# Performance work log

Measured on AMD Instinct MI355X. Metric: run time of the kernel, lower is better.

## Reference

```python
import jax, jax.numpy as jnp
import numpy as np

DIM = 1024
DEPTH = 3
BATCH = 8
SEQ = DIM  # module requires seq_len == dim for the residual add to broadcast


def setup_inputs() -> dict:
    key = jax.random.key(0)
    k1, k2, k3, k4 = jax.random.split(key, 4)
    x = jax.random.normal(k1, (BATCH, SEQ, DIM), dtype=jnp.float32)
    # torch.nn.Linear(dim, 3*dim): weight [3*dim, dim], bias [3*dim]
    Wqkv = jax.random.normal(k2, (3 * DIM, DIM), dtype=jnp.float32) * (1.0 / np.sqrt(DIM))
    bqkv = jax.random.normal(k3, (3 * DIM,), dtype=jnp.float32) * 0.01
    # self.w: Parameter of shape [depth, dim, dim], init randn
    w = jax.random.normal(k4, (DEPTH, DIM, DIM), dtype=jnp.float32)
    return {"x": x, "Wqkv": Wqkv, "bqkv": bqkv, "w": w}


def reference(x, Wqkv, bqkv, w):
    # qkv projection then chunk into q, k, v along last dim
    qkv = x @ Wqkv.T + bqkv                      # [B, S, 3*dim]
    q, k, v = jnp.split(qkv, 3, axis=-1)         # each [B, S, dim]
    scale = 1.0 / (q.shape[-1] ** 0.5)
    # sum over depth of (q @ w[i]) @ k^T, accumulated onto v
    # einsum contracts d (dim), e (dim), and sums over n (depth) in one pass
    scores = jnp.einsum('bsd,nde,bte->bst', q, w, k)  # [B, S, S]; requires S == dim
    return v + scores * scale
```

## Files before the change

kernel.cpp:

```cpp
#include <hip/hip_runtime.h>
#include <hip/hip_bf16.h>
#include <stdint.h>

typedef __bf16 bf16_t;
typedef __bf16 bf16x8 __attribute__((ext_vector_type(8)));
typedef __bf16 bf16x4 __attribute__((ext_vector_type(4)));
typedef float  f32x4  __attribute__((ext_vector_type(4)));

#define DIM   1024
#define BATCH 8
#define SCALE 0.03125f


__device__ __forceinline__ float rowdot_bf16(const bf16_t* __restrict__ row,
                                             const float* __restrict__ vec, int lane) {
    float s = 0.f;
#pragma unroll
    for (int c = 0; c < 2; ++c) {
        const int d0 = (lane + c * 64) * 8;
        const bf16x8 v = *reinterpret_cast<const bf16x8*>(row + d0);
#pragma unroll
        for (int e = 0; e < 8; ++e) s += vec[d0 + e] * (float)v[e];
    }
#pragma unroll
    for (int off = 32; off; off >>= 1) s += __shfl_down(s, off);
    return s;
}

__device__ __forceinline__ void cvt4(const float* __restrict__ in,
                                     bf16_t* __restrict__ out, int i) {
    const float4 v = reinterpret_cast<const float4*>(in)[i];
    bf16x4 o;
    o.x = (bf16_t)v.x; o.y = (bf16_t)v.y; o.z = (bf16_t)v.z; o.w = (bf16_t)v.w;
    reinterpret_cast<bf16x4*>(out)[i] = o;
}

__device__ __forceinline__ void gemm_sk(const bf16_t* __restrict__ A, const bf16_t* __restrict__ B,
                                        float* __restrict__ oP, int s, int tid,
                                        bf16_t* As, bf16_t* Bs)
{
    const int wave = tid >> 6, lane = tid & 63;
    const int bm = (s >> 5) * 128;
    const int bn = ((s >> 2) & 7) * 128;
    const int kb = (s & 3) * 256;
    float* outP  = oP + (long)(s & 3) * 1048576;
    const int wr = wave >> 1, wc = wave & 1;
    const int lhi = lane >> 4, llo = lane & 15;

    f32x4 acc[4][4];
    const f32x4 fz = {0.f, 0.f, 0.f, 0.f};
#pragma unroll
    for (int i = 0; i < 4; ++i)
#pragma unroll
        for (int j = 0; j < 4; ++j) acc[i][j] = fz;

    for (int k0 = 0; k0 < 256; k0 += 32) {
#pragma unroll
        for (int i = 0; i < 2; ++i) {
            const int c  = wave * 128 + i * 64 + lane;
            const int r  = c >> 2;
            const int cc = (c & 3) << 3;
            const long ga = (long)(bm + r) * 1024 + kb + k0 + cc;
            const long gb = (long)(bn + r) * 1024 + kb + k0 + cc;
            const int lbase = (wave * 128 + i * 64) << 3;
            __builtin_amdgcn_global_load_lds(
                (const __attribute__((address_space(1))) uint32_t*)(A + ga),
                (__attribute__((address_space(3))) uint32_t*)(&As[lbase]), 16, 0, 0);
            __builtin_amdgcn_global_load_lds(
                (const __attribute__((address_space(1))) uint32_t*)(B + gb),
                (__attribute__((address_space(3))) uint32_t*)(&Bs[lbase]), 16, 0, 0);
        }
        __syncthreads();

        bf16x8 af[4], bfr[4];
#pragma unroll
        for (int mi = 0; mi < 4; ++mi)
            af[mi] = *reinterpret_cast<const bf16x8*>(&As[(wr * 64 + mi * 16 + llo) * 32 + lhi * 8]);
#pragma unroll
        for (int ni = 0; ni < 4; ++ni)
            bfr[ni] = *reinterpret_cast<const bf16x8*>(&Bs[(wc * 64 + ni * 16 + llo) * 32 + lhi * 8]);
#pragma unroll
        for (int mi = 0; mi < 4; ++mi)
#pragma unroll
            for (int ni = 0; ni < 4; ++ni)
                acc[mi][ni] = __builtin_amdgcn_mfma_f32_16x16x32_bf16(af[mi], bfr[ni], acc[mi][ni], 0, 0, 0);
        __syncthreads();
    }

#pragma unroll
    for (int mi = 0; mi < 4; ++mi) {
        const int r0 = bm + wr * 64 + mi * 16 + lhi * 4;
#pragma unroll
        for (int ni = 0; ni < 4; ++ni) {
            const int cg = bn + wc * 64 + ni * 16 + llo;
            const f32x4 v = acc[mi][ni];
#pragma unroll
            for (int j = 0; j < 4; ++j)
                outP[(long)(r0 + j) * 1024 + cg] = v[j];
        }
    }
}

__global__ __launch_bounds__(256)
void k_prep(const float* __restrict__ Wqkv, const float* __restrict__ w,
            bf16_t* __restrict__ weff, bf16_t* __restrict__ wtb,
            bf16_t* __restrict__ wqt, bf16_t* __restrict__ wkt)
{
    __shared__ float tile[32][33];
    const int b = blockIdx.x;
    if (b < 1024) {
        const int t  = b;
        const int tx = threadIdx.x & 31, ty = threadIdx.x >> 5;
        const int d0 = (t & 31) * 32, e0 = (t >> 5) * 32;
#pragma unroll
        for (int r = 0; r < 4; ++r) {
            const int d = d0 + r * 8 + ty;
            const int e = e0 + tx;
            const float sum =
                w[d * 1024 + e] + w[1048576 + d * 1024 + e] + w[2097152 + d * 1024 + e];
            tile[r * 8 + ty][tx] = sum;
            weff[(long)d * 1024 + e] = (bf16_t)sum;
        }
        __syncthreads();
#pragma unroll
        for (int r = 0; r < 4; ++r) {
            const int e = e0 + r * 8 + ty;
            const int d = d0 + tx;
            wtb[(long)e * 1024 + d] = (bf16_t)tile[tx][r * 8 + ty];
        }
    } else {
        const bool isQ = (b < 2048);
        const int t  = b - (isQ ? 1024 : 2048);
        const float* src = isQ ? Wqkv : (Wqkv + 1048576);
        bf16_t* dst = isQ ? wqt : wkt;
        const int tx = threadIdx.x & 31, ty = threadIdx.x >> 5;
        const int e0 = (t & 31) * 32, d0 = (t >> 5) * 32;
#pragma unroll
        for (int r = 0; r < 4; ++r)
            tile[r * 8 + ty][tx] = src[(long)(e0 + r * 8 + ty) * 1024 + d0 + tx];
        __syncthreads();
#pragma unroll
        for (int r = 0; r < 4; ++r)
            dst[(long)(d0 + r * 8 + ty) * 1024 + e0 + tx] = (bf16_t)tile[tx][r * 8 + ty];
    }
}

__global__ __launch_bounds__(256)
void k_midA(const bf16_t* __restrict__ wkt, const bf16_t* __restrict__ weff,
            const bf16_t* __restrict__ wtb, const float* __restrict__ bqkv,
            const float* __restrict__ x, bf16_t* __restrict__ xb,
            float* __restrict__ pX1, float* __restrict__ h1, float* __restrict__ h2)
{
    __shared__ __align__(16) bf16_t As[128 * 32];
    __shared__ __align__(16) bf16_t Bs[128 * 32];
    const int b = blockIdx.x;
    if (b < 256) {
        gemm_sk(wkt, weff, pX1, b, threadIdx.x, As, Bs);
        return;
    }
    if (b < 768) {
        const int wave = threadIdx.x >> 6, lane = threadIdx.x & 63;
        const int r = (b - 256) * 4 + wave;
        if (r < 1024) {
            const float s = rowdot_bf16(weff + (long)r * 1024, bqkv + 1024, lane);
            if (lane == 0) h1[r] = s;
        } else {
            const float s = rowdot_bf16(wtb + (long)(r - 1024) * 1024, bqkv, lane);
            if (lane == 0) h2[r - 1024] = s;
        }
        return;
    }
    cvt4(x, xb, (b - 768) * 256 + threadIdx.x);
}

__global__ __launch_bounds__(256)
void k_cvtA(const float* __restrict__ p, bf16_t* __restrict__ X1b,
            const bf16_t* __restrict__ wqt, const bf16_t* __restrict__ wkt,
            const float* __restrict__ h1, const float* __restrict__ h2,
            const float* __restrict__ bqkv,
            float* __restrict__ u, float* __restrict__ w2, float* __restrict__ cO)
{
    const int b = blockIdx.x;
    if (b < 1024) {
        const int i = b * 256 + threadIdx.x;
        const f32x4* rp = reinterpret_cast<const f32x4*>(p);
        const f32x4 a0 = rp[i], a1 = rp[i + 262144], a2 = rp[i + 524288], a3 = rp[i + 786432];
        bf16x4 o;
        o.x = (bf16_t)(a0.x + a1.x + a2.x + a3.x);
        o.y = (bf16_t)(a0.y + a1.y + a2.y + a3.y);
        o.z = (bf16_t)(a0.z + a1.z + a2.z + a3.z);
        o.w = (bf16_t)(a0.w + a1.w + a2.w + a3.w);
        reinterpret_cast<bf16x4*>(X1b)[i] = o;
    } else if (b < 1536) {
        const int wave = threadIdx.x >> 6, lane = threadIdx.x & 63;
        const int rr = (b - 1024) * 4 + wave;
        if (rr < 1024) {
            const float s = rowdot_bf16(wqt + (long)rr * 1024, h1, lane);
            if (lane == 0) u[rr] = s;
        } else {
            const float s = rowdot_bf16(wkt + (long)(rr - 1024) * 1024, h2, lane);
            if (lane == 0) w2[rr - 1024] = s;
        }
    } else {
        if (threadIdx.x < 64) {
            float s = 0.f;
            for (int i = threadIdx.x; i < 1024; i += 64) s += bqkv[i] * h1[i];
#pragma unroll
            for (int off = 32; off; off >>= 1) s += __shfl_down(s, off);
            if (threadIdx.x == 0) cO[0] = s;
        }
    }
}

__global__ __launch_bounds__(256)
void k_midB(const bf16_t* __restrict__ X1b, const bf16_t* __restrict__ wqt,
            float* __restrict__ pMT, const bf16_t* __restrict__ xb,
            const float* __restrict__ u, const float* __restrict__ w2,
            const float* __restrict__ cO, const float* __restrict__ Wqkv,
            bf16_t* __restrict__ wvb,
            float* __restrict__ RU, float* __restrict__ RW)
{
    __shared__ __align__(16) bf16_t As[128 * 32];
    __shared__ __align__(16) bf16_t Bs[128 * 32];
    const int b = blockIdx.x;
    if (b < 256) {
        gemm_sk(X1b, wqt, pMT, b, threadIdx.x, As, Bs);
        return;
    }
    if (b < 2304) {
        const int wave = threadIdx.x >> 6, lane = threadIdx.x & 63;
        const int s = (b - 256) * 4 + wave;
        const bf16_t* row = xb + (long)s * 1024;
        float s1 = 0.f, s2 = 0.f;
#pragma unroll
        for (int c = 0; c < 2; ++c) {
            const int d0 = (lane + c * 64) * 8;
            const bf16x8 v = *reinterpret_cast<const bf16x8*>(row + d0);
#pragma unroll
            for (int e = 0; e < 8; ++e) {
                const float f = (float)v[e];
                s1 += u[d0 + e] * f;
                s2 += w2[d0 + e] * f;
            }
        }
#pragma unroll
        for (int off = 32; off; off >>= 1) { s1 += __shfl_down(s1, off); s2 += __shfl_down(s2, off); }
        if (lane == 0) {
            RU[s] = SCALE * (s1 + cO[0]);
            RW[s] = SCALE * s2;
        }
        return;
    }
    cvt4(Wqkv + 2097152, wvb, (b - 2304) * 256 + threadIdx.x);
}

__global__ __launch_bounds__(256)
void k_cvtS(const float* __restrict__ p, bf16_t* __restrict__ out) {
    const int i = blockIdx.x * 256 + threadIdx.x;
    const f32x4* rp = reinterpret_cast<const f32x4*>(p);
    const f32x4 a0 = rp[i], a1 = rp[i + 262144], a2 = rp[i + 524288], a3 = rp[i + 786432];
    bf16x4 o;
    o.x = (bf16_t)(SCALE * (a0.x + a1.x + a2.x + a3.x));
    o.y = (bf16_t)(SCALE * (a0.y + a1.y + a2.y + a3.y));
    o.z = (bf16_t)(SCALE * (a0.z + a1.z + a2.z + a3.z));
    o.w = (bf16_t)(SCALE * (a0.w + a1.w + a2.w + a3.w));
    reinterpret_cast<bf16x4*>(out)[i] = o;
}

#define GLOAD(SRC, DST) __builtin_amdgcn_global_load_lds( \
    (const __attribute__((address_space(1))) uint32_t*)(SRC), \
    (__attribute__((address_space(3))) uint32_t*)(DST), 16, 0, 0)

template<int MODE>
__global__ __launch_bounds__(512, 2)
void k_db2(const bf16_t* __restrict__ A1, const bf16_t* __restrict__ A2,
           const bf16_t* __restrict__ B1, const bf16_t* __restrict__ B2,
           const float* __restrict__ RUv, const float* __restrict__ RWv,
           const float* __restrict__ bv,
           bf16_t* __restrict__ oT, float* __restrict__ oF)
{
    constexpr int SLOT = 32768;
    constexpr int NTT  = (MODE == 0) ? 16 : 32;
    __shared__ __align__(16) unsigned char slds[2 * SLOT];

    const int tid  = threadIdx.x;
    const int wave = tid >> 6, lane = tid & 63;
    const int wm = wave >> 2, wn = wave & 3;
    const int llo = lane & 15, lhi = lane >> 4;

    int bm, bn, z = 0;
    const int nw = ((int)blockIdx.x & 7) * 64 + ((int)blockIdx.x >> 3);
    if (MODE == 0) {
        bm = (nw >> 3) * 128;
        bn = (nw & 7) * 128;
    } else {
        z = nw >> 6;
        const int r = nw & 63;
        bm = (r >> 3) * 128; bn = (r & 7) * 128;
    }
    const long zo = (long)z << 20;

    const bf16_t *sA1[2], *sB1[2], *sA2[2], *sB2[2];
    int dA[2], dB[2];
#pragma unroll
    for (int j = 0; j < 2; ++j) {
        const int C = j * 512 + tid;
        const int r = C >> 3, u = (C & 7) ^ (r & 7);
        const long aoff = (long)(bm + r) * 1024 + (u << 3);
        const long boff = (long)(bn + r) * 1024 + (u << 3);
        sA1[j] = A1 + zo + aoff;  dA[j] = C << 4;
        sB1[j] = B1 + zo + boff;  dB[j] = 16384 + (C << 4);
        if (MODE == 1) { sA2[j] = A2 + zo + aoff; sB2[j] = B2 + boff; }
    }

    auto stage = [&](int tt) {
        unsigned char* s = &slds[(tt & 1) * SLOT];
        const long ko = (long)(tt & 15) << 6;
        const bool hB = (MODE == 1) && (tt >= 16);
#pragma unroll
        for (int j = 0; j < 2; ++j) {
            GLOAD((hB ? sA2[j] : sA1[j]) + ko, s + dA[j]);
            GLOAD((hB ? sB2[j] : sB1[j]) + ko, s + dB[j]);
        }
    };

    f32x4 acc[4][2];
    const f32x4 fz = {0.f, 0.f, 0.f, 0.f};
#pragma unroll
    for (int i = 0; i < 4; ++i)
#pragma unroll
        for (int j = 0; j < 2; ++j) acc[i][j] = fz;

    stage(0);

    for (int t = 0; t < NTT; ++t) {
        if (t + 1 < NTT) {
            stage(t + 1);
            asm volatile("s_waitcnt vmcnt(4)" ::: "memory");
        } else {
            asm volatile("s_waitcnt vmcnt(0)" ::: "memory");
        }
        __builtin_amdgcn_s_barrier();

        const unsigned char* sb = &slds[(t & 1) * SLOT];
#pragma unroll
        for (int ks = 0; ks < 2; ++ks) {
            bf16x8 af[4], bfv[2];
#pragma unroll
            for (int mi = 0; mi < 4; ++mi) {
                const int r = wm * 64 + mi * 16 + llo;
                af[mi] = *reinterpret_cast<const bf16x8*>(
                    sb + r * 128 + ((((ks << 2) | lhi) ^ (r & 7)) << 4));
            }
#pragma unroll
            for (int ni = 0; ni < 2; ++ni) {
                const int r = wn * 32 + ni * 16 + llo;
                bfv[ni] = *reinterpret_cast<const bf16x8*>(
                    sb + 16384 + r * 128 + ((((ks << 2) | lhi) ^ (r & 7)) << 4));
            }
            __builtin_amdgcn_s_setprio(1);
#pragma unroll
            for (int mi = 0; mi < 4; ++mi)
#pragma unroll
                for (int ni = 0; ni < 2; ++ni)
                    acc[mi][ni] = __builtin_amdgcn_mfma_f32_16x16x32_bf16(
                        af[mi], bfv[ni], acc[mi][ni], 0, 0, 0);
            __builtin_amdgcn_s_setprio(0);
        }
        asm volatile("s_waitcnt lgkmcnt(0)" ::: "memory");
        __builtin_amdgcn_s_barrier();
    }

#pragma unroll
    for (int mi = 0; mi < 4; ++mi) {
        const int lr0 = bm + wm * 64 + mi * 16 + lhi * 4;
#pragma unroll
        for (int ni = 0; ni < 2; ++ni) {
            const int cg = bn + wn * 32 + ni * 16 + llo;
            const f32x4 v = acc[mi][ni];
            if (MODE == 0) {
#pragma unroll
                for (int j = 0; j < 4; ++j)
                    oT[(long)(lr0 + j) * 1024 + cg] = (bf16_t)v[j];
            } else {
                const float cterm = RWv[z * 1024 + cg] + bv[cg];
#pragma unroll
                for (int j = 0; j < 4; ++j) {
                    const int lr = lr0 + j;
                    oF[zo + (long)lr * 1024 + cg] = v[j] + RUv[z * 1024 + lr] + cterm;
                }
            }
        }
    }
}
#undef GLOAD

extern "C" void kernel_launch(void* const* d_in, const int* in_sizes, int n_in,
                              void* d_out, int out_size, void* d_ws, size_t ws_size,
                              hipStream_t stream) {
    const float* x    = (const float*)d_in[0];
    const float* Wqkv = (const float*)d_in[1];
    const float* bqkv = (const float*)d_in[2];
    const float* w    = (const float*)d_in[3];
    float* out = (float*)d_out;

    char* ws = (char*)d_ws;
    bf16_t* xb   = (bf16_t*)ws;
    float*  pbig = (float*) (ws + (16l << 20));
    bf16_t* tsb  = (bf16_t*)(ws + (16l << 20));
    bf16_t* weff = (bf16_t*)(ws + (32l << 20));
    bf16_t* wtb  = (bf16_t*)(ws + (34l << 20));
    bf16_t* wqt  = (bf16_t*)(ws + (36l << 20));
    bf16_t* wkt  = (bf16_t*)(ws + (38l << 20));
    bf16_t* wvb  = (bf16_t*)(ws + (40l << 20));
    bf16_t* X1b  = (bf16_t*)(ws + (42l << 20));
    bf16_t* MTb  = (bf16_t*)(ws + (44l << 20));
    char*   sm   = ws + (46l << 20);
    float* h1 = (float*)sm;
    float* h2 = (float*)(sm + 4096);
    float* u  = (float*)(sm + 8192);
    float* w2 = (float*)(sm + 12288);
    float* cO = (float*)(sm + 16384);
    float* RU = (float*)(sm + 20480);
    float* RW = (float*)(sm + 53248);
    if (ws_size < (size_t)(54l << 20) + 65536) return;

    k_prep<<<3072, 256, 0, stream>>>(Wqkv, w, weff, wtb, wqt, wkt);

    k_midA<<<8960, 256, 0, stream>>>(wkt, weff, wtb, bqkv, x, xb, pbig, h1, h2);

    k_cvtA<<<1537, 256, 0, stream>>>(pbig, X1b, wqt, wkt, h1, h2, bqkv, u, w2, cO);

    k_midB<<<3328, 256, 0, stream>>>(X1b, wqt, pbig, xb, u, w2, cO, Wqkv, wvb, RU, RW);

    k_cvtS<<<1024, 256, 0, stream>>>(pbig, MTb);

    k_db2<0><<<512, 512, 0, stream>>>(xb, nullptr, MTb, nullptr,
                                      nullptr, nullptr, nullptr, tsb, nullptr);

    k_db2<1><<<512, 512, 0, stream>>>(tsb, xb, xb, wvb,
                                      RU, RW, bqkv + 2048, nullptr, out);
}
```

Measured before the change: 107.7 us.

## Merge five prep kernels into one cooperative persistent kernel with grid syncs

Replaces the k_prep, k_midA, k_cvtA, k_midB and k_cvtS launches with a single 256-block cooperative kernel. Each block loops over its share of the work, and grid.sync() separates the dependent phases. This removes four kernel launch gaps and their tail effects. The cost is lower parallelism in the elementwise and transpose phases, which previously used thousands of blocks, plus the overhead of each grid barrier.

After: 238.6 us. 2.22x slower.

```diff
diff --git a/kernel.cpp b/kernel.cpp
--- a/kernel.cpp
+++ b/kernel.cpp
@@ -1,6 +1,9 @@
 #include <hip/hip_runtime.h>
 #include <hip/hip_bf16.h>
+#include <hip/hip_cooperative_groups.h>
 #include <stdint.h>
+
+namespace cg = cooperative_groups;
 
 typedef __bf16 bf16_t;
 typedef __bf16 bf16x8 __attribute__((ext_vector_type(8)));
@@ -101,313 +104,12 @@
     }
 }
 
-__global__ __launch_bounds__(256)
-void k_prep(const float* __restrict__ Wqkv, const float* __restrict__ w,
-            bf16_t* __restrict__ weff, bf16_t* __restrict__ wtb,
-            bf16_t* __restrict__ wqt, bf16_t* __restrict__ wkt)
+__global__ __launch_bounds__(256, 2)
+void k_chain(const float* x, const float* Wqkv, const float* w,
+             const float* bqkv, char* ws)
 {
-    __shared__ float tile[32][33];
-    const int b = blockIdx.x;
-    if (b < 1024) {
-        const int t  = b;
-        const int tx = threadIdx.x & 31, ty = threadIdx.x >> 5;
-        const int d0 = (t & 31) * 32, e0 = (t >> 5) * 32;
-#pragma unroll
-        for (int r = 0; r < 4; ++r) {
-            const int d = d0 + r * 8 + ty;
-            const int e = e0 + tx;
-            const float sum =
-                w[d * 1024 + e] + w[1048576 + d * 1024 + e] + w[2097152 + d * 1024 + e];
-            tile[r * 8 + ty][tx] = sum;
-            weff[(long)d * 1024 + e] = (bf16_t)sum;
-        }
-        __syncthreads();
-#pragma unroll
-        for (int r = 0; r < 4; ++r) {
-            const int e = e0 + r * 8 + ty;
-            const int d = d0 + tx;
-            wtb[(long)e * 1024 + d] = (bf16_t)tile[tx][r * 8 + ty];
-        }
-    } else {
-        const bool isQ = (b < 2048);
-        const int t  = b - (isQ ? 1024 : 2048);
-        const float* src = isQ ? Wqkv : (Wqkv + 1048576);
-        bf16_t* dst = isQ ? wqt : wkt;
-        const int tx = threadIdx.x & 31, ty = threadIdx.x >> 5;
-        const int e0 = (t & 31) * 32, d0 = (t >> 5) * 32;
-#pragma unroll
-        for (int r = 0; r < 4; ++r)
-            tile[r * 8 + ty][tx] = src[(long)(e0 + r * 8 + ty) * 1024 + d0 + tx];
-        __syncthreads();
-#pragma unroll
-        for (int r = 0; r < 4; ++r)
-            dst[(long)(d0 + r * 8 + ty) * 1024 + e0 + tx] = (bf16_t)tile[tx][r * 8 + ty];
-    }
-}
-
-__global__ __launch_bounds__(256)
-void k_midA(const bf16_t* __restrict__ wkt, const bf16_t* __restrict__ weff,
-            const bf16_t* __restrict__ wtb, const float* __restrict__ bqkv,
-            const float* __restrict__ x, bf16_t* __restrict__ xb,
-            float* __restrict__ pX1, float* __restrict__ h1, float* __restrict__ h2)
-{
-    __shared__ __align__(16) bf16_t As[128 * 32];
-    __shared__ __align__(16) bf16_t Bs[128 * 32];
-    const int b = blockIdx.x;
-    if (b < 256) {
-        gemm_sk(wkt, weff, pX1, b, threadIdx.x, As, Bs);
-        return;
-    }
-    if (b < 768) {
-        const int wave = threadIdx.x >> 6, lane = threadIdx.x & 63;
-        const int r = (b - 256) * 4 + wave;
-        if (r < 1024) {
-            const float s = rowdot_bf16(weff + (long)r * 1024, bqkv + 1024, lane);
-            if (lane == 0) h1[r] = s;
-        } else {
-            const float s = rowdot_bf16(wtb + (long)(r - 1024) * 1024, bqkv, lane);
-            if (lane == 0) h2[r - 1024] = s;
-        }
-        return;
-    }
-    cvt4(x, xb, (b - 768) * 256 + threadIdx.x);
-}
-
-__global__ __launch_bounds__(256)
-void k_cvtA(const float* __restrict__ p, bf16_t* __restrict__ X1b,
-            const bf16_t* __restrict__ wqt, const bf16_t* __restrict__ wkt,
-            const float* __restrict__ h1, const float* __restrict__ h2,
-            const float* __restrict__ bqkv,
-            float* __restrict__ u, float* __restrict__ w2, float* __restrict__ cO)
-{
-    const int b = blockIdx.x;
-    if (b < 1024) {
-        const int i = b * 256 + threadIdx.x;
-        const f32x4* rp = reinterpret_cast<const f32x4*>(p);
-        const f32x4 a0 = rp[i], a1 = rp[i + 262144], a2 = rp[i + 524288], a3 = rp[i + 786432];
-        bf16x4 o;
-        o.x = (bf16_t)(a0.x + a1.x + a2.x + a3.x);
-        o.y = (bf16_t)(a0.y + a1.y + a2.y + a3.y);
-        o.z = (bf16_t)(a0.z + a1.z + a2.z + a3.z);
-        o.w = (bf16_t)(a0.w + a1.w + a2.w + a3.w);
-        reinterpret_cast<bf16x4*>(X1b)[i] = o;
-    } else if (b < 1536) {
-        const int wave = threadIdx.x >> 6, lane = threadIdx.x & 63;
-        const int rr = (b - 1024) * 4 + wave;
-        if (rr < 1024) {
-            const float s = rowdot_bf16(wqt + (long)rr * 1024, h1, lane);
-            if (lane == 0) u[rr] = s;
-        } else {
-            const float s = rowdot_bf16(wkt + (long)(rr - 1024) * 1024, h2, lane);
-            if (lane == 0) w2[rr - 1024] = s;
-        }
-    } else {
-        if (threadIdx.x < 64) {
-            float s = 0.f;
-            for (int i = threadIdx.x; i < 1024; i += 64) s += bqkv[i] * h1[i];
-#pragma unroll
-            for (int off = 32; off; off >>= 1) s += __shfl_down(s, off);
-            if (threadIdx.x == 0) cO[0] = s;
-        }
-    }
-}
-
-__global__ __launch_bounds__(256)
-void k_midB(const bf16_t* __restrict__ X1b, const bf16_t* __restrict__ wqt,
-            float* __restrict__ pMT, const bf16_t* __restrict__ xb,
-            const float* __restrict__ u, const float* __restrict__ w2,
-            const float* __restrict__ cO, const float* __restrict__ Wqkv,
-            bf16_t* __restrict__ wvb,
-            float* __restrict__ RU, float* __restrict__ RW)
-{
-    __shared__ __align__(16) bf16_t As[128 * 32];
-    __shared__ __align__(16) bf16_t Bs[128 * 32];
-    const int b = blockIdx.x;
-    if (b < 256) {
-        gemm_sk(X1b, wqt, pMT, b, threadIdx.x, As, Bs);
-        return;
-    }
-    if (b < 2304) {
-        const int wave = threadIdx.x >> 6, lane = threadIdx.x & 63;
-        const int s = (b - 256) * 4 + wave;
-        const bf16_t* row = xb + (long)s * 1024;
-        float s1 = 0.f, s2 = 0.f;
-#pragma unroll
-        for (int c = 0; c < 2; ++c) {
-            const int d0 = (lane + c * 64) * 8;
-            const bf16x8 v = *reinterpret_cast<const bf16x8*>(row + d0);
-#pragma unroll
-            for (int e = 0; e < 8; ++e) {
-                const float f = (float)v[e];
-                s1 += u[d0 + e] * f;
-                s2 += w2[d0 + e] * f;
-            }
-        }
-#pragma unroll
-        for (int off = 32; off; off >>= 1) { s1 += __shfl_down(s1, off); s2 += __shfl_down(s2, off); }
-        if (lane == 0) {
-            RU[s] = SCALE * (s1 + cO[0]);
-            RW[s] = SCALE * s2;
-        }
-        return;
-    }
-    cvt4(Wqkv + 2097152, wvb, (b - 2304) * 256 + threadIdx.x);
-}
-
-__global__ __launch_bounds__(256)
-void k_cvtS(const float* __restrict__ p, bf16_t* __restrict__ out) {
-    const int i = blockIdx.x * 256 + threadIdx.x;
-    const f32x4* rp = reinterpret_cast<const f32x4*>(p);
-    const f32x4 a0 = rp[i], a1 = rp[i + 262144], a2 = rp[i + 524288], a3 = rp[i + 786432];
-    bf16x4 o;
-    o.x = (bf16_t)(SCALE * (a0.x + a1.x + a2.x + a3.x));
-    o.y = (bf16_t)(SCALE * (a0.y + a1.y + a2.y + a3.y));
-    o.z = (bf16_t)(SCALE * (a0.z + a1.z + a2.z + a3.z));
-    o.w = (bf16_t)(SCALE * (a0.w + a1.w + a2.w + a3.w));
-    reinterpret_cast<bf16x4*>(out)[i] = o;
-}
-
-#define GLOAD(SRC, DST) __builtin_amdgcn_global_load_lds( \
-    (const __attribute__((address_space(1))) uint32_t*)(SRC), \
-    (__attribute__((address_space(3))) uint32_t*)(DST), 16, 0, 0)
-
-template<int MODE>
-__global__ __launch_bounds__(512, 2)
-void k_db2(const bf16_t* __restrict__ A1, const bf16_t* __restrict__ A2,
-           const bf16_t* __restrict__ B1, const bf16_t* __restrict__ B2,
-           const float* __restrict__ RUv, const float* __restrict__ RWv,
-           const float* __restrict__ bv,
-           bf16_t* __restrict__ oT, float* __restrict__ oF)
-{
-    constexpr int SLOT = 32768;
-    constexpr int NTT  = (MODE == 0) ? 16 : 32;
-    __shared__ __align__(16) unsigned char slds[2 * SLOT];
-
-    const int tid  = threadIdx.x;
-    const int wave = tid >> 6, lane = tid & 63;
-    const int wm = wave >> 2, wn = wave & 3;
-    const int llo = lane & 15, lhi = lane >> 4;
-
-    int bm, bn, z = 0;
-    const int nw = ((int)blockIdx.x & 7) * 64 + ((int)blockIdx.x >> 3);
-    if (MODE == 0) {
-        bm = (nw >> 3) * 128;
-        bn = (nw & 7) * 128;
-    } else {
-        z = nw >> 6;
-        const int r = nw & 63;
-        bm = (r >> 3) * 128; bn = (r & 7) * 128;
-    }
-    const long zo = (long)z << 20;
-
-    const bf16_t *sA1[2], *sB1[2], *sA2[2], *sB2[2];
-    int dA[2], dB[2];
-#pragma unroll
-    for (int j = 0; j < 2; ++j) {
-        const int C = j * 512 + tid;
-        const int r = C >> 3, u = (C & 7) ^ (r & 7);
-        const long aoff = (long)(bm + r) * 1024 + (u << 3);
-        const long boff = (long)(bn + r) * 1024 + (u << 3);
-        sA1[j] = A1 + zo + aoff;  dA[j] = C << 4;
-        sB1[j] = B1 + zo + boff;  dB[j] = 16384 + (C << 4);
-        if (MODE == 1) { sA2[j] = A2 + zo + aoff; sB2[j] = B2 + boff; }
-    }
-
-    auto stage = [&](int tt) {
-        unsigned char* s = &slds[(tt & 1) * SLOT];
-        const long ko = (long)(tt & 15) << 6;
-        const bool hB = (MODE == 1) && (tt >= 16);
-#pragma unroll
-        for (int j = 0; j < 2; ++j) {
-            GLOAD((hB ? sA2[j] : sA1[j]) + ko, s + dA[j]);
-            GLOAD((hB ? sB2[j] : sB1[j]) + ko, s + dB[j]);
-        }
-    };
-
-    f32x4 acc[4][2];
-    const f32x4 fz = {0.f, 0.f, 0.f, 0.f};
-#pragma unroll
-    for (int i = 0; i < 4; ++i)
-#pragma unroll
-        for (int j = 0; j < 2; ++j) acc[i][j] = fz;
-
-    stage(0);
-
-    for (int t = 0; t < NTT; ++t) {
-        if (t + 1 < NTT) {
-            stage(t + 1);
-            asm volatile("s_waitcnt vmcnt(4)" ::: "memory");
-        } else {
-            asm volatile("s_waitcnt vmcnt(0)" ::: "memory");
-        }
-        __builtin_amdgcn_s_barrier();
-
-        const unsigned char* sb = &slds[(t & 1) * SLOT];
-#pragma unroll
-        for (int ks = 0; ks < 2; ++ks) {
-            bf16x8 af[4], bfv[2];
-#pragma unroll
-            for (int mi = 0; mi < 4; ++mi) {
-                const int r = wm * 64 + mi * 16 + llo;
-                af[mi] = *reinterpret_cast<const bf16x8*>(
-                    sb + r * 128 + ((((ks << 2) | lhi) ^ (r & 7)) << 4));
-            }
-#pragma unroll
-            for (int ni = 0; ni < 2; ++ni) {
-                const int r = wn * 32 + ni * 16 + llo;
-                bfv[ni] = *reinterpret_cast<const bf16x8*>(
-                    sb + 16384 + r * 128 + ((((ks << 2) | lhi) ^ (r & 7)) << 4));
-            }
-            __builtin_amdgcn_s_setprio(1);
-#pragma unroll
-            for (int mi = 0; mi < 4; ++mi)
-#pragma unroll
-                for (int ni = 0; ni < 2; ++ni)
-                    acc[mi][ni] = __builtin_amdgcn_mfma_f32_16x16x32_bf16(
-                        af[mi], bfv[ni], acc[mi][ni], 0, 0, 0);
-            __builtin_amdgcn_s_setprio(0);
-        }
-        asm volatile("s_waitcnt lgkmcnt(0)" ::: "memory");
-        __builtin_amdgcn_s_barrier();
-    }
-
-#pragma unroll
-    for (int mi = 0; mi < 4; ++mi) {
-        const int lr0 = bm + wm * 64 + mi * 16 + lhi * 4;
-#pragma unroll
-        for (int ni = 0; ni < 2; ++ni) {
-            const int cg = bn + wn * 32 + ni * 16 + llo;
-            const f32x4 v = acc[mi][ni];
-            if (MODE == 0) {
-#pragma unroll
-                for (int j = 0; j < 4; ++j)
-                    oT[(long)(lr0 + j) * 1024 + cg] = (bf16_t)v[j];
-            } else {
-                const float cterm = RWv[z * 1024 + cg] + bv[cg];
-#pragma unroll
-                for (int j = 0; j < 4; ++j) {
-                    const int lr = lr0 + j;
-                    oF[zo + (long)lr * 1024 + cg] = v[j] + RUv[z * 1024 + lr] + cterm;
-                }
-            }
-        }
-    }
-}
-#undef GLOAD
-
-extern "C" void kernel_launch(void* const* d_in, const int* in_sizes, int n_in,
-                              void* d_out, int out_size, void* d_ws, size_t ws_size,
-                              hipStream_t stream) {
-    const float* x    = (const float*)d_in[0];
-    const float* Wqkv = (const float*)d_in[1];
-    const float* bqkv = (const float*)d_in[2];
-    const float* w    = (const float*)d_in[3];
-    float* out = (float*)d_out;
-
-    char* ws = (char*)d_ws;
     bf16_t* xb   = (bf16_t*)ws;
     float*  pbig = (float*) (ws + (16l << 20));
-    bf16_t* tsb  = (bf16_t*)(ws + (16l << 20));
     bf16_t* weff = (bf16_t*)(ws + (32l << 20));
     bf16_t* wtb  = (bf16_t*)(ws + (34l << 20));
     bf16_t* wqt  = (bf16_t*)(ws + (36l << 20));
@@ -423,17 +125,296 @@
     float* cO = (float*)(sm + 16384);
     float* RU = (float*)(sm + 20480);
     float* RW = (float*)(sm + 53248);
+
+    __shared__ float tile[32][33];
+    __shared__ __align__(16) bf16_t As[128 * 32];
+    __shared__ __align__(16) bf16_t Bs[128 * 32];
+
+    cg::grid_group grid = cg::this_grid();
+    const int b = blockIdx.x, tid = threadIdx.x;
+    const int wave = tid >> 6, lane = tid & 63;
+    const int tx = tid & 31, ty = tid >> 5;
+
+#pragma unroll 1
+    for (int it = 0; it < 12; ++it) {
+        const int t = b * 12 + it;
+        if (t < 1024) {
+            const int d0 = (t & 31) * 32, e0 = (t >> 5) * 32;
+#pragma unroll
+            for (int r = 0; r < 4; ++r) {
+                const int d = d0 + r * 8 + ty;
+                const int e = e0 + tx;
+                const float sum =
+                    w[d * 1024 + e] + w[1048576 + d * 1024 + e] + w[2097152 + d * 1024 + e];
+                tile[r * 8 + ty][tx] = sum;
+                weff[(long)d * 1024 + e] = (bf16_t)sum;
+            }
+            __syncthreads();
+#pragma unroll
+            for (int r = 0; r < 4; ++r) {
+                const int e = e0 + r * 8 + ty;
+                const int d = d0 + tx;
+                wtb[(long)e * 1024 + d] = (bf16_t)tile[tx][r * 8 + ty];
+            }
+            __syncthreads();
+        } else {
+            const bool isQ = (t < 2048);
+            const int tt = t - (isQ ? 1024 : 2048);
+            const float* src = isQ ? Wqkv : (Wqkv + 1048576);
+            bf16_t* dst = isQ ? wqt : wkt;
+            const int e0 = (tt & 31) * 32, d0 = (tt >> 5) * 32;
+#pragma unroll
+            for (int r = 0; r < 4; ++r)
+                tile[r * 8 + ty][tx] = src[(long)(e0 + r * 8 + ty) * 1024 + d0 + tx];
+            __syncthreads();
+#pragma unroll
+            for (int r = 0; r < 4; ++r)
+                dst[(long)(d0 + r * 8 + ty) * 1024 + e0 + tx] = (bf16_t)tile[tx][r * 8 + ty];
+            __syncthreads();
+        }
+    }
+#pragma unroll 1
+    for (int it = 0; it < 32; ++it) cvt4(x, xb, (b * 32 + it) * 256 + tid);
+#pragma unroll 1
+    for (int it = 0; it < 4; ++it)  cvt4(Wqkv + 2097152, wvb, (b * 4 + it) * 256 + tid);
+    grid.sync();
+
+    gemm_sk(wkt, weff, pbig, b, tid, As, Bs);
+#pragma unroll 1
+    for (int it = 0; it < 2; ++it) {
+        const int r = b * 8 + wave + 4 * it;
+        if (r < 1024) {
+            const float s = rowdot_bf16(weff + (long)r * 1024, bqkv + 1024, lane);
+            if (lane == 0) h1[r] = s;
+        } else {
+            const float s = rowdot_bf16(wtb + (long)(r - 1024) * 1024, bqkv, lane);
+            if (lane == 0) h2[r - 1024] = s;
+        }
+    }
+    grid.sync();
+
+#pragma unroll 1
+    for (int it = 0; it < 4; ++it) {
+        const int i = (b * 4 + it) * 256 + tid;
+        const f32x4* rp = reinterpret_cast<const f32x4*>(pbig);
+        const f32x4 a0 = rp[i], a1 = rp[i + 262144], a2 = rp[i + 524288], a3 = rp[i + 786432];
+        bf16x4 o;
+        o.x = (bf16_t)(a0.x + a1.x + a2.x + a3.x);
+        o.y = (bf16_t)(a0.y + a1.y + a2.y + a3.y);
+        o.z = (bf16_t)(a0.z + a1.z + a2.z + a3.z);
+        o.w = (bf16_t)(a0.w + a1.w + a2.w + a3.w);
+        reinterpret_cast<bf16x4*>(X1b)[i] = o;
+    }
+#pragma unroll 1
+    for (int it = 0; it < 2; ++it) {
+        const int rr = b * 8 + wave + 4 * it;
+        if (rr < 1024) {
+            const float s = rowdot_bf16(wqt + (long)rr * 1024, h1, lane);
+            if (lane == 0) u[rr] = s;
+        } else {
+            const float s = rowdot_bf16(wkt + (long)(rr - 1024) * 1024, h2, lane);
+            if (lane == 0) w2[rr - 1024] = s;
+        }
+    }
+    if (b == 0 && tid < 64) {
+        float s = 0.f;
+        for (int i = tid; i < 1024; i += 64) s += bqkv[i] * h1[i];
+#pragma unroll
+        for (int off = 32; off; off >>= 1) s += __shfl_down(s, off);
+        if (tid == 0) cO[0] = s;
+    }
+    grid.sync();
+
+    gemm_sk(X1b, wqt, pbig, b, tid, As, Bs);
+#pragma unroll 1
+    for (int it = 0; it < 8; ++it) {
+        const int s = b * 32 + wave + 4 * it;
+        const bf16_t* row = xb + (long)s * 1024;
+        float s1 = 0.f, s2 = 0.f;
+#pragma unroll
+        for (int c = 0; c < 2; ++c) {
+            const int d0 = (lane + c * 64) * 8;
+            const bf16x8 v = *reinterpret_cast<const bf16x8*>(row + d0);
+#pragma unroll
+            for (int e = 0; e < 8; ++e) {
+                const float f = (float)v[e];
+                s1 += u[d0 + e] * f;
+                s2 += w2[d0 + e] * f;
+            }
+        }
+#pragma unroll
+        for (int off = 32; off; off >>= 1) { s1 += __shfl_down(s1, off); s2 += __shfl_down(s2, off); }
+        if (lane == 0) {
+            RU[s] = SCALE * (s1 + cO[0]);
+            RW[s] = SCALE * s2;
+        }
+    }
+    grid.sync();
+
+#pragma unroll 1
+    for (int it = 0; it < 4; ++it) {
+        const int i = (b * 4 + it) * 256 + tid;
+        const f32x4* rp = reinterpret_cast<const f32x4*>(pbig);
+        const f32x4 a0 = rp[i], a1 = rp[i + 262144], a2 = rp[i + 524288], a3 = rp[i + 786432];
+        bf16x4 o;
+        o.x = (bf16_t)(SCALE * (a0.x + a1.x + a2.x + a3.x));
+        o.y = (bf16_t)(SCALE * (a0.y + a1.y + a2.y + a3.y));
+        o.z = (bf16_t)(SCALE * (a0.z + a1.z + a2.z + a3.z));
+        o.w = (bf16_t)(SCALE * (a0.w + a1.w + a2.w + a3.w));
+        reinterpret_cast<bf16x4*>(MTb)[i] = o;
+    }
+}
+
+#define GLOAD(SRC, DST) __builtin_amdgcn_global_load_lds( \
+    (const __attribute__((address_space(1))) uint32_t*)(SRC), \
+    (__attribute__((address_space(3))) uint32_t*)(DST), 16, 0, 0)
+
+template<int MODE>
+__global__ __launch_bounds__(512, 2)
+void k_db2(const bf16_t* __restrict__ A1, const bf16_t* __restrict__ A2,
+           const bf16_t* __restrict__ B1, const bf16_t* __restrict__ B2,
+           const float* __restrict__ RUv, const float* __restrict__ RWv,
+           const float* __restrict__ bv,
+           bf16_t* __restrict__ oT, float* __restrict__ oF)
+{
+    constexpr int SLOT = 32768;
+    constexpr int NTT  = (MODE == 0) ? 16 : 32;
+    __shared__ __align__(16) unsigned char slds[2 * SLOT];
+
+    const int tid  = threadIdx.x;
+    const int wave = tid >> 6, lane = tid & 63;
+    const int wm = wave >> 2, wn = wave & 3;
+    const int llo = lane & 15, lhi = lane >> 4;
+
+    int bm, bn, z = 0;
+    const int nw = ((int)blockIdx.x & 7) * 64 + ((int)blockIdx.x >> 3);
+    if (MODE == 0) {
+        bm = (nw >> 3) * 128;
+        bn = (nw & 7) * 128;
+    } else {
+        z = nw >> 6;
+        const int r = nw & 63;
+        bm = (r >> 3) * 128; bn = (r & 7) * 128;
+    }
+    const long zo = (long)z << 20;
+
+    const bf16_t *sA1[2], *sB1[2], *sA2[2], *sB2[2];
+    int dA[2], dB[2];
+#pragma unroll
+    for (int j = 0; j < 2; ++j) {
+        const int C = j * 512 + tid;
+        const int r = C >> 3, u = (C & 7) ^ (r & 7);
+        const long aoff = (long)(bm + r) * 1024 + (u << 3);
+        const long boff = (long)(bn + r) * 1024 + (u << 3);
+        sA1[j] = A1 + zo + aoff;  dA[j] = C << 4;
+        sB1[j] = B1 + zo + boff;  dB[j] = 16384 + (C << 4);
+        if (MODE == 1) { sA2[j] = A2 + zo + aoff; sB2[j] = B2 + boff; }
+    }
+
+    auto stage = [&](int tt) {
+        unsigned char* s = &slds[(tt & 1) * SLOT];
+        const long ko = (long)(tt & 15) << 6;
+        const bool hB = (MODE == 1) && (tt >= 16);
+#pragma unroll
+        for (int j = 0; j < 2; ++j) {
+            GLOAD((hB ? sA2[j] : sA1[j]) + ko, s + dA[j]);
+            GLOAD((hB ? sB2[j] : sB1[j]) + ko, s + dB[j]);
+        }
+    };
+
+    f32x4 acc[4][2];
+    const f32x4 fz = {0.f, 0.f, 0.f, 0.f};
+#pragma unroll
+    for (int i = 0; i < 4; ++i)
+#pragma unroll
+        for (int j = 0; j < 2; ++j) acc[i][j] = fz;
+
+    stage(0);
+
+    for (int t = 0; t < NTT; ++t) {
+        if (t + 1 < NTT) {
+            stage(t + 1);
+            asm volatile("s_waitcnt vmcnt(4)" ::: "memory");
+        } else {
+            asm volatile("s_waitcnt vmcnt(0)" ::: "memory");
+        }
+        __builtin_amdgcn_s_barrier();
+
+        const unsigned char* sb = &slds[(t & 1) * SLOT];
+#pragma unroll
+        for (int ks = 0; ks < 2; ++ks) {
+            bf16x8 af[4], bfv[2];
+#pragma unroll
+            for (int mi = 0; mi < 4; ++mi) {
+                const int r = wm * 64 + mi * 16 + llo;
+                af[mi] = *reinterpret_cast<const bf16x8*>(
+                    sb + r * 128 + ((((ks << 2) | lhi) ^ (r & 7)) << 4));
+            }
+#pragma unroll
+            for (int ni = 0; ni < 2; ++ni) {
+                const int r = wn * 32 + ni * 16 + llo;
+                bfv[ni] = *reinterpret_cast<const bf16x8*>(
+                    sb + 16384 + r * 128 + ((((ks << 2) | lhi) ^ (r & 7)) << 4));
+            }
+            __builtin_amdgcn_s_setprio(1);
+#pragma unroll
+            for (int mi = 0; mi < 4; ++mi)
+#pragma unroll
+                for (int ni = 0; ni < 2; ++ni)
+                    acc[mi][ni] = __builtin_amdgcn_mfma_f32_16x16x32_bf16(
+                        af[mi], bfv[ni], acc[mi][ni], 0, 0, 0);
+            __builtin_amdgcn_s_setprio(0);
+        }
+        asm volatile("s_waitcnt lgkmcnt(0)" ::: "memory");
+        __builtin_amdgcn_s_barrier();
+    }
+
+#pragma unroll
+    for (int mi = 0; mi < 4; ++mi) {
+        const int lr0 = bm + wm * 64 + mi * 16 + lhi * 4;
+#pragma unroll
+        for (int ni = 0; ni < 2; ++ni) {
+            const int cg = bn + wn * 32 + ni * 16 + llo;
+            const f32x4 v = acc[mi][ni];
+            if (MODE == 0) {
+#pragma unroll
+                for (int j = 0; j < 4; ++j)
+                    oT[(long)(lr0 + j) * 1024 + cg] = (bf16_t)v[j];
+            } else {
+                const float cterm = RWv[z * 1024 + cg] + bv[cg];
+#pragma unroll
+                for (int j = 0; j < 4; ++j) {
+                    const int lr = lr0 + j;
+                    oF[zo + (long)lr * 1024 + cg] = v[j] + RUv[z * 1024 + lr] + cterm;
+                }
+            }
+        }
+    }
+}
+#undef GLOAD
+
+extern "C" void kernel_launch(void* const* d_in, const int* in_sizes, int n_in,
+                              void* d_out, int out_size, void* d_ws, size_t ws_size,
+                              hipStream_t stream) {
+    const float* x    = (const float*)d_in[0];
+    const float* Wqkv = (const float*)d_in[1];
+    const float* bqkv = (const float*)d_in[2];
+    const float* w    = (const float*)d_in[3];
+    float* out = (float*)d_out;
+
+    char* wsb = (char*)d_ws;
+    bf16_t* xb   = (bf16_t*)wsb;
+    bf16_t* tsb  = (bf16_t*)(wsb + (16l << 20));
+    bf16_t* wvb  = (bf16_t*)(wsb + (40l << 20));
+    bf16_t* MTb  = (bf16_t*)(wsb + (44l << 20));
+    char*   sm   = wsb + (46l << 20);
+    float* RU = (float*)(sm + 20480);
+    float* RW = (float*)(sm + 53248);
     if (ws_size < (size_t)(54l << 20) + 65536) return;
 
-    k_prep<<<3072, 256, 0, stream>>>(Wqkv, w, weff, wtb, wqt, wkt);
-
-    k_midA<<<8960, 256, 0, stream>>>(wkt, weff, wtb, bqkv, x, xb, pbig, h1, h2);
-
-    k_cvtA<<<1537, 256, 0, stream>>>(pbig, X1b, wqt, wkt, h1, h2, bqkv, u, w2, cO);
-
-    k_midB<<<3328, 256, 0, stream>>>(X1b, wqt, pbig, xb, u, w2, cO, Wqkv, wvb, RU, RW);
-
-    k_cvtS<<<1024, 256, 0, stream>>>(pbig, MTb);
+    void* args[] = { (void*)&x, (void*)&Wqkv, (void*)&w, (void*)&bqkv, (void*)&wsb };
+    hipLaunchCooperativeKernel(reinterpret_cast<void*>(k_chain),
+                               dim3(256), dim3(256), args, 0, stream);
 
     k_db2<0><<<512, 512, 0, stream>>>(xb, nullptr, MTb, nullptr,
                                       nullptr, nullptr, nullptr, tsb, nullptr);
```
